# Performance work log

Measured on AMD Instinct MI355X. Metric: run time of the kernel, lower is better.

## Reference

```python
import jax, jax.numpy as jnp
import numpy as np

N_NODES = 100000
N_EDGES = 1000000
D_IN = 256
D_OUT = 64


def setup_inputs() -> dict:
    key = jax.random.key(0)
    k1, k2, k3, k4, k5, k6 = jax.random.split(key, 6)
    x = jax.random.normal(k1, (N_NODES, D_IN), dtype=jnp.float32)
    # Xavier-style uniform init: stdv = 1/sqrt(output_dim)
    stdv = 1.0 / np.sqrt(D_OUT)
    weight = jax.random.uniform(k2, (D_IN, D_OUT), dtype=jnp.float32, minval=-stdv, maxval=stdv)
    adj_vals = jax.random.uniform(k3, (N_EDGES,), dtype=jnp.float32)
    prelu_a = jnp.full((1,), 0.25, dtype=jnp.float32)  # nn.PReLU default
    row = jax.random.randint(k4, (N_EDGES,), 0, N_NODES, dtype=jnp.int32)
    col = jax.random.randint(k5, (N_EDGES,), 0, N_NODES, dtype=jnp.int32)
    return {"x": x, "weight": weight, "adj_vals": adj_vals, "prelu_a": prelu_a,
            "row": row, "col": col}


def reference(x, weight, adj_vals, prelu_a, row, col):
    # dense GEMM: [N, D_in] @ [D_in, D_out]
    hidden = x @ weight  # gc_drop=0 -> identity dropout
    # sparse adj spmm: out[i] = sum_{e: row[e]=i} adj_vals[e] * hidden[col[e]]
    msg = adj_vals[:, None] * hidden[col]  # [E, D_out]
    agg = jax.ops.segment_sum(msg, row, num_segments=N_NODES)  # [N, D_out]
    # PReLU with single shared slope
    out = jnp.where(agg > 0, agg, prelu_a * agg)
    return out
```

## Files before the change

kernel.cpp:

```cpp
#include <hip/hip_runtime.h>

#define N_NODES 100000
#define N_EDGES 1000000
#define D_IN    256
#define D_OUT   64

#define BKT_SHIFT   5
#define NODES_PER_BKT 32
#define N_BKT       3125
#define BKT_CAP     512

#define EPB         2048
#define BIN_BLOCKS  489
#define GEMM_BLOCKS 782
#define NUM_TILES   6250
#define AGG_BLOCKS  391

typedef __attribute__((ext_vector_type(8))) short short8;
typedef __attribute__((ext_vector_type(4))) float f32x4;

__device__ __forceinline__ unsigned short f2bf(float f) {
    unsigned int u = __float_as_uint(f);
    u = (u + 0x7fffu + ((u >> 16) & 1u)) >> 16;
    return (unsigned short)u;
}

__device__ __forceinline__ void mfma_store_tile(
    const short8 afrag[8], const unsigned short wT[64][272],
    unsigned short* __restrict__ hiddenBf, int r0, int n16, int quad)
{
    f32x4 acc[4] = {{0.f,0.f,0.f,0.f},{0.f,0.f,0.f,0.f},
                    {0.f,0.f,0.f,0.f},{0.f,0.f,0.f,0.f}};
#pragma unroll
    for (int ct = 0; ct < 4; ++ct) {
#pragma unroll
        for (int kk = 0; kk < 8; ++kk) {
            short8 b = *(const short8*)&wT[ct * 16 + n16][kk * 32 + quad * 8];
            acc[ct] = __builtin_amdgcn_mfma_f32_16x16x32_bf16(
                afrag[kk], b, acc[ct], 0, 0, 0);
        }
    }
#pragma unroll
    for (int ct = 0; ct < 4; ++ct)
#pragma unroll
        for (int reg = 0; reg < 4; ++reg)
            hiddenBf[(size_t)(r0 + quad * 4 + reg) * D_OUT + ct * 16 + n16]
                = f2bf(acc[ct][reg]);
}

__global__ __launch_bounds__(256, 2) void bin_kernel(
    const int* __restrict__ row, const int* __restrict__ col,
    const float* __restrict__ adj, int* __restrict__ gCursor,
    int2* __restrict__ edges)
{
    __shared__ int cnt[N_BKT];
    __shared__ int cbase[N_BKT];
    __shared__ int cur[N_BKT];

    const int t  = threadIdx.x;
    const int e0 = blockIdx.x * EPB;

    for (int i = t; i < N_BKT; i += 256) cnt[i] = 0;
    __syncthreads();

    int rreg[8];
#pragma unroll
    for (int u = 0; u < 8; ++u) {
        int e = e0 + t + u * 256;
        rreg[u] = (e < N_EDGES) ? row[e] : -1;
    }
#pragma unroll
    for (int u = 0; u < 8; ++u)
        if (rreg[u] >= 0) atomicAdd(&cnt[rreg[u] >> BKT_SHIFT], 1);
    __syncthreads();

    for (int i = t; i < N_BKT; i += 256) {
        int c = cnt[i];
        cbase[i] = c ? atomicAdd(&gCursor[i], c) : 0;
        cur[i] = 0;
    }
    __syncthreads();

    int cc[8]; float vv[8];
#pragma unroll
    for (int u = 0; u < 8; ++u) {
        int e = e0 + t + u * 256;
        if (rreg[u] >= 0) { cc[u] = col[e]; vv[u] = adj[e]; }
        else              { cc[u] = 0;      vv[u] = 0.f;    }
    }
#pragma unroll
    for (int u = 0; u < 8; ++u) {
        int r = rreg[u];
        if (r >= 0) {
            int b = r >> BKT_SHIFT;
            int off = cbase[b] + atomicAdd(&cur[b], 1);
            if (off < BKT_CAP) {
                edges[b * BKT_CAP + off] =
                    make_int2(((r & (NODES_PER_BKT - 1)) << 17) | cc[u],
                              __float_as_int(vv[u]));
            }
        }
    }
}

__global__ __launch_bounds__(256, 2) void gemm_kernel(
    const float* __restrict__ x, const float* __restrict__ w,
    unsigned short* __restrict__ hiddenBf)
{
    const int t = threadIdx.x;

    __shared__ unsigned short wT[64][272];

    for (int i = 0; i < 64; ++i) {
        int idx = t + i * 256;
        int k = idx >> 6, n = idx & 63;
        wT[n][k] = f2bf(w[idx]);
    }
    __syncthreads();

    const int lane = t & 63;
    const int wid  = t >> 6;
    const int n16  = lane & 15;
    const int quad = lane >> 4;

    const int waveGid = blockIdx.x * 4 + wid;
    const int t0 = waveGid * 2;
    if (t0 >= NUM_TILES) return;

    float4 lo[8], hi[8];
    short8 afrag[8];

    {
        const float* xrow = x + (size_t)(t0 * 16 + n16) * D_IN + quad * 8;
#pragma unroll
        for (int kk = 0; kk < 8; ++kk) {
            lo[kk] = *(const float4*)(xrow + kk * 32);
            hi[kk] = *(const float4*)(xrow + kk * 32 + 4);
        }
    }
#pragma unroll
    for (int kk = 0; kk < 8; ++kk) {
        short8 a;
        a[0] = (short)f2bf(lo[kk].x); a[1] = (short)f2bf(lo[kk].y);
        a[2] = (short)f2bf(lo[kk].z); a[3] = (short)f2bf(lo[kk].w);
        a[4] = (short)f2bf(hi[kk].x); a[5] = (short)f2bf(hi[kk].y);
        a[6] = (short)f2bf(hi[kk].z); a[7] = (short)f2bf(hi[kk].w);
        afrag[kk] = a;
    }

    const int t1 = t0 + 1;
    const bool have1 = t1 < NUM_TILES;
    if (have1) {
        const float* xrow = x + (size_t)(t1 * 16 + n16) * D_IN + quad * 8;
#pragma unroll
        for (int kk = 0; kk < 8; ++kk) {
            lo[kk] = *(const float4*)(xrow + kk * 32);
            hi[kk] = *(const float4*)(xrow + kk * 32 + 4);
        }
    }

    mfma_store_tile(afrag, wT, hiddenBf, t0 * 16, n16, quad);

    if (have1) {
#pragma unroll
        for (int kk = 0; kk < 8; ++kk) {
            short8 a;
            a[0] = (short)f2bf(lo[kk].x); a[1] = (short)f2bf(lo[kk].y);
            a[2] = (short)f2bf(lo[kk].z); a[3] = (short)f2bf(lo[kk].w);
            a[4] = (short)f2bf(hi[kk].x); a[5] = (short)f2bf(hi[kk].y);
            a[6] = (short)f2bf(hi[kk].z); a[7] = (short)f2bf(hi[kk].w);
            afrag[kk] = a;
        }
        mfma_store_tile(afrag, wT, hiddenBf, t1 * 16, n16, quad);
    }
}

__global__ __launch_bounds__(512, 2) void bucket_agg_kernel(
    const unsigned short* __restrict__ hiddenBf,
    const int2* __restrict__ edges, const int* __restrict__ gCursor,
    const float* __restrict__ prelu_a, float* __restrict__ out)
{
    __shared__ float acc[8][NODES_PER_BKT * D_OUT];

    const int t      = threadIdx.x;
    const int lane   = t & 63;
    const int wid    = t >> 6;
    const int bucket = blockIdx.x * 8 + wid;
    if (bucket >= N_BKT) return;

    float* A = acc[wid];

    float4* A4 = (float4*)A;
#pragma unroll
    for (int i = 0; i < 8; ++i)
        A4[lane + i * 64] = make_float4(0.f, 0.f, 0.f, 0.f);

    const int base = bucket * BKT_CAP;
    int size = gCursor[bucket];
    if (size > BKT_CAP) size = BKT_CAP;

    for (int i0 = 0; i0 < size; i0 += 64) {
        int take = size - i0;
        if (take > 64) take = 64;
        int2 rec = make_int2(0, 0);
        if (lane < take) rec = edges[base + i0 + lane];

        int j = 0;
        for (; j + 16 <= take; j += 16) {
            int nl[16]; int c[16]; float v[16]; float h[16];
#pragma unroll
            for (int u = 0; u < 16; ++u) {
                int rx = __builtin_amdgcn_readlane(rec.x, j + u);
                nl[u] = (unsigned)rx >> 17;
                c[u]  = rx & 0x1FFFF;
                v[u]  = __int_as_float(__builtin_amdgcn_readlane(rec.y, j + u));
            }
#pragma unroll
            for (int u = 0; u < 16; ++u)
                h[u] = __uint_as_float(
                    (unsigned)hiddenBf[(size_t)c[u] * D_OUT + lane] << 16);
#pragma unroll
            for (int u = 0; u < 16; ++u)
                A[nl[u] * D_OUT + lane] += v[u] * h[u];
        }
        for (; j + 8 <= take; j += 8) {
            int nl[8]; int c[8]; float v[8]; float h[8];
#pragma unroll
            for (int u = 0; u < 8; ++u) {
                int rx = __builtin_amdgcn_readlane(rec.x, j + u);
                nl[u] = (unsigned)rx >> 17;
                c[u]  = rx & 0x1FFFF;
                v[u]  = __int_as_float(__builtin_amdgcn_readlane(rec.y, j + u));
            }
#pragma unroll
            for (int u = 0; u < 8; ++u)
                h[u] = __uint_as_float(
                    (unsigned)hiddenBf[(size_t)c[u] * D_OUT + lane] << 16);
#pragma unroll
            for (int u = 0; u < 8; ++u)
                A[nl[u] * D_OUT + lane] += v[u] * h[u];
        }
        for (; j < take; ++j) {
            int rx  = __builtin_amdgcn_readlane(rec.x, j);
            float v = __int_as_float(__builtin_amdgcn_readlane(rec.y, j));
            float h = __uint_as_float(
                (unsigned)hiddenBf[(size_t)(rx & 0x1FFFF) * D_OUT + lane] << 16);
            A[((unsigned)rx >> 17) * D_OUT + lane] += v * h;
        }
    }

    const float a = prelu_a[0];
    const int node0 = bucket * NODES_PER_BKT;
#pragma unroll
    for (int i = 0; i < NODES_PER_BKT; ++i) {
        float s = A[i * D_OUT + lane];
        out[(size_t)(node0 + i) * D_OUT + lane] = s > 0.f ? s : a * s;
    }
}

extern "C" void kernel_launch(void* const* d_in, const int* in_sizes, int n_in,
                              void* d_out, int out_size, void* d_ws, size_t ws_size,
                              hipStream_t stream)
{
    const float* x       = (const float*)d_in[0];
    const float* w       = (const float*)d_in[1];
    const float* adj     = (const float*)d_in[2];
    const float* prelu_a = (const float*)d_in[3];
    const int*   row     = (const int*)d_in[4];
    const int*   col     = (const int*)d_in[5];
    float* out = (float*)d_out;

    char* ws = (char*)d_ws;
    unsigned short* hiddenBf = (unsigned short*)(ws);
    int2*  edges    = (int2*)        (ws + 12800000);
    int*   gCursor  = (int*)         (ws + 25600000);

    hipMemsetAsync(gCursor, 0, N_BKT * sizeof(int), stream);

    bin_kernel<<<BIN_BLOCKS, 256, 0, stream>>>(row, col, adj, gCursor, edges);

    gemm_kernel<<<GEMM_BLOCKS, 256, 0, stream>>>(x, w, hiddenBf);

    bucket_agg_kernel<<<AGG_BLOCKS, 512, 0, stream>>>(
        hiddenBf, edges, gCursor, prelu_a, out);
}
```

Baseline: 251.9 us.

## Aggregate buckets with MFMA one-hot matmul and fold cursor reset into GEMM

Replaces the per-edge LDS scalar accumulation with a matrix-core formulation. Each wave gathers 32 neighbour rows of bf16 hidden into a transposed LDS tile, builds a one-hot 16x32 edge-to-node matrix holding the edge weight, and accumulates with MFMA. The weight is split into hi and lo bf16 parts to keep precision, which doubles the MFMA count. Buckets shrink to 16 nodes to fit the 16-row MFMA tile. The cursor memset is replaced by zeroing inside the GEMM kernel, which is now launched first.

After: 240.3 us. 4.6% less time.

```diff
diff --git a/kernel.cpp b/kernel.cpp
--- a/kernel.cpp
+++ b/kernel.cpp
@@ -5,19 +5,19 @@
 #define D_IN    256
 #define D_OUT   64
 
-#define BKT_SHIFT   5
-#define NODES_PER_BKT 32
-#define N_BKT       3125
-#define BKT_CAP     512
-
+#define BKT_SHIFT   4
+#define NODES_PER_BKT 16
+#define N_BKT       6250
+#define BKT_CAP     256
 #define EPB         2048
 #define BIN_BLOCKS  489
 #define GEMM_BLOCKS 782
 #define NUM_TILES   6250
-#define AGG_BLOCKS  391
+#define AGG_BLOCKS  782
 
 typedef __attribute__((ext_vector_type(8))) short short8;
 typedef __attribute__((ext_vector_type(4))) float f32x4;
+typedef __attribute__((ext_vector_type(4))) unsigned short u16x4;
 
 __device__ __forceinline__ unsigned short f2bf(float f) {
     unsigned int u = __float_as_uint(f);
@@ -48,66 +48,15 @@
                 = f2bf(acc[ct][reg]);
 }
 
-__global__ __launch_bounds__(256, 2) void bin_kernel(
-    const int* __restrict__ row, const int* __restrict__ col,
-    const float* __restrict__ adj, int* __restrict__ gCursor,
-    int2* __restrict__ edges)
-{
-    __shared__ int cnt[N_BKT];
-    __shared__ int cbase[N_BKT];
-    __shared__ int cur[N_BKT];
-
-    const int t  = threadIdx.x;
-    const int e0 = blockIdx.x * EPB;
-
-    for (int i = t; i < N_BKT; i += 256) cnt[i] = 0;
-    __syncthreads();
-
-    int rreg[8];
-#pragma unroll
-    for (int u = 0; u < 8; ++u) {
-        int e = e0 + t + u * 256;
-        rreg[u] = (e < N_EDGES) ? row[e] : -1;
-    }
-#pragma unroll
-    for (int u = 0; u < 8; ++u)
-        if (rreg[u] >= 0) atomicAdd(&cnt[rreg[u] >> BKT_SHIFT], 1);
-    __syncthreads();
-
-    for (int i = t; i < N_BKT; i += 256) {
-        int c = cnt[i];
-        cbase[i] = c ? atomicAdd(&gCursor[i], c) : 0;
-        cur[i] = 0;
-    }
-    __syncthreads();
-
-    int cc[8]; float vv[8];
-#pragma unroll
-    for (int u = 0; u < 8; ++u) {
-        int e = e0 + t + u * 256;
-        if (rreg[u] >= 0) { cc[u] = col[e]; vv[u] = adj[e]; }
-        else              { cc[u] = 0;      vv[u] = 0.f;    }
-    }
-#pragma unroll
-    for (int u = 0; u < 8; ++u) {
-        int r = rreg[u];
-        if (r >= 0) {
-            int b = r >> BKT_SHIFT;
-            int off = cbase[b] + atomicAdd(&cur[b], 1);
-            if (off < BKT_CAP) {
-                edges[b * BKT_CAP + off] =
-                    make_int2(((r & (NODES_PER_BKT - 1)) << 17) | cc[u],
-                              __float_as_int(vv[u]));
-            }
-        }
-    }
-}
-
 __global__ __launch_bounds__(256, 2) void gemm_kernel(
     const float* __restrict__ x, const float* __restrict__ w,
-    unsigned short* __restrict__ hiddenBf)
+    unsigned short* __restrict__ hiddenBf, int* __restrict__ gCursor)
 {
     const int t = threadIdx.x;
+
+    if (blockIdx.x == 0) {
+        for (int i = t; i < N_BKT; i += 256) gCursor[i] = 0;
+    }
 
     __shared__ unsigned short wT[64][272];
 
@@ -175,25 +124,84 @@
     }
 }
 
-__global__ __launch_bounds__(512, 2) void bucket_agg_kernel(
+__global__ __launch_bounds__(256, 2) void bin_kernel(
+    const int* __restrict__ row, const int* __restrict__ col,
+    const float* __restrict__ adj, int* __restrict__ gCursor,
+    int2* __restrict__ edges)
+{
+    __shared__ int cnt[N_BKT];
+    __shared__ int cbase[N_BKT];
+    __shared__ int cur[N_BKT];
+
+    const int t  = threadIdx.x;
+    const int e0 = blockIdx.x * EPB;
+
+    for (int i = t; i < N_BKT; i += 256) cnt[i] = 0;
+    __syncthreads();
+
+    int rreg[8];
+#pragma unroll
+    for (int u = 0; u < 8; ++u) {
+        int e = e0 + t + u * 256;
+        rreg[u] = (e < N_EDGES) ? row[e] : -1;
+    }
+#pragma unroll
+    for (int u = 0; u < 8; ++u)
+        if (rreg[u] >= 0) atomicAdd(&cnt[rreg[u] >> BKT_SHIFT], 1);
+    __syncthreads();
+
+    for (int i = t; i < N_BKT; i += 256) {
+        int c = cnt[i];
+        cbase[i] = c ? atomicAdd(&gCursor[i], c) : 0;
+        cur[i] = 0;
+    }
+    __syncthreads();
+
+    int cc[8]; float vv[8];
+#pragma unroll
+    for (int u = 0; u < 8; ++u) {
+        int e = e0 + t + u * 256;
+        if (rreg[u] >= 0) { cc[u] = col[e]; vv[u] = adj[e]; }
+        else              { cc[u] = 0;      vv[u] = 0.f;    }
+    }
+#pragma unroll
+    for (int u = 0; u < 8; ++u) {
+        int r = rreg[u];
+        if (r >= 0) {
+            int b = r >> BKT_SHIFT;
+            int off = cbase[b] + atomicAdd(&cur[b], 1);
+            if (off < BKT_CAP) {
+                unsigned hi = f2bf(vv[u]);
+                float hif  = __uint_as_float(hi << 16);
+                unsigned lo = f2bf(vv[u] - hif);
+                edges[b * BKT_CAP + off] =
+                    make_int2(((r & (NODES_PER_BKT - 1)) << 17) | cc[u],
+                              (int)((hi << 16) | lo));
+            }
+        }
+    }
+}
+
+__global__ __launch_bounds__(512) void agg_mfma_kernel(
     const unsigned short* __restrict__ hiddenBf,
     const int2* __restrict__ edges, const int* __restrict__ gCursor,
     const float* __restrict__ prelu_a, float* __restrict__ out)
 {
-    __shared__ float acc[8][NODES_PER_BKT * D_OUT];
-
-    const int t      = threadIdx.x;
-    const int lane   = t & 63;
-    const int wid    = t >> 6;
+    __shared__ unsigned short hT[8][64][40];
+
+    const int t    = threadIdx.x;
+    const int lane = t & 63;
+    const int wid  = t >> 6;
     const int bucket = blockIdx.x * 8 + wid;
     if (bucket >= N_BKT) return;
 
-    float* A = acc[wid];
-
-    float4* A4 = (float4*)A;
-#pragma unroll
-    for (int i = 0; i < 8; ++i)
-        A4[lane + i * 64] = make_float4(0.f, 0.f, 0.f, 0.f);
+    const int n16  = lane & 15;
+    const int quad = lane >> 4;
+
+    unsigned short (*H)[40] = hT[wid];
+
+    f32x4 acc[4] = {{0.f,0.f,0.f,0.f},{0.f,0.f,0.f,0.f},
+                    {0.f,0.f,0.f,0.f},{0.f,0.f,0.f,0.f}};
 
     const int base = bucket * BKT_CAP;
     int size = gCursor[bucket];
@@ -205,57 +213,59 @@
         int2 rec = make_int2(0, 0);
         if (lane < take) rec = edges[base + i0 + lane];
 
-        int j = 0;
-        for (; j + 16 <= take; j += 16) {
-            int nl[16]; int c[16]; float v[16]; float h[16];
-#pragma unroll
-            for (int u = 0; u < 16; ++u) {
-                int rx = __builtin_amdgcn_readlane(rec.x, j + u);
-                nl[u] = (unsigned)rx >> 17;
-                c[u]  = rx & 0x1FFFF;
-                v[u]  = __int_as_float(__builtin_amdgcn_readlane(rec.y, j + u));
-            }
-#pragma unroll
-            for (int u = 0; u < 16; ++u)
-                h[u] = __uint_as_float(
-                    (unsigned)hiddenBf[(size_t)c[u] * D_OUT + lane] << 16);
-#pragma unroll
-            for (int u = 0; u < 16; ++u)
-                A[nl[u] * D_OUT + lane] += v[u] * h[u];
-        }
-        for (; j + 8 <= take; j += 8) {
-            int nl[8]; int c[8]; float v[8]; float h[8];
-#pragma unroll
-            for (int u = 0; u < 8; ++u) {
-                int rx = __builtin_amdgcn_readlane(rec.x, j + u);
-                nl[u] = (unsigned)rx >> 17;
-                c[u]  = rx & 0x1FFFF;
-                v[u]  = __int_as_float(__builtin_amdgcn_readlane(rec.y, j + u));
-            }
-#pragma unroll
-            for (int u = 0; u < 8; ++u)
-                h[u] = __uint_as_float(
-                    (unsigned)hiddenBf[(size_t)c[u] * D_OUT + lane] << 16);
-#pragma unroll
-            for (int u = 0; u < 8; ++u)
-                A[nl[u] * D_OUT + lane] += v[u] * h[u];
-        }
-        for (; j < take; ++j) {
-            int rx  = __builtin_amdgcn_readlane(rec.x, j);
-            float v = __int_as_float(__builtin_amdgcn_readlane(rec.y, j));
-            float h = __uint_as_float(
-                (unsigned)hiddenBf[(size_t)(rx & 0x1FFFF) * D_OUT + lane] << 16);
-            A[((unsigned)rx >> 17) * D_OUT + lane] += v * h;
+#pragma unroll
+        for (int s = 0; s < 2; ++s) {
+#pragma unroll
+            for (int g = 0; g < 2; ++g) {
+                int cc[16]; unsigned short hh[16];
+#pragma unroll
+                for (int u = 0; u < 16; ++u)
+                    cc[u] = __builtin_amdgcn_readlane(rec.x, s * 32 + g * 16 + u)
+                            & 0x1FFFF;
+#pragma unroll
+                for (int u = 0; u < 16; ++u)
+                    hh[u] = hiddenBf[(size_t)cc[u] * D_OUT + lane];
+#pragma unroll
+                for (int u = 0; u < 16; u += 4) {
+                    u16x4 p;
+                    p[0] = hh[u]; p[1] = hh[u + 1];
+                    p[2] = hh[u + 2]; p[3] = hh[u + 3];
+                    *(u16x4*)&H[lane][g * 16 + u] = p;
+                }
+            }
+
+            short8 ahi, alo;
+#pragma unroll
+            for (int j = 0; j < 8; ++j) {
+                int e  = s * 32 + quad * 8 + j;
+                int rx = __shfl(rec.x, e);
+                int ry = __shfl(rec.y, e);
+                bool m = (((unsigned)rx >> 17) == (unsigned)n16);
+                ahi[j] = m ? (short)((unsigned)ry >> 16) : (short)0;
+                alo[j] = m ? (short)(ry & 0xFFFF)        : (short)0;
+            }
+
+#pragma unroll
+            for (int ct = 0; ct < 4; ++ct) {
+                short8 b = *(const short8*)&H[ct * 16 + n16][quad * 8];
+                acc[ct] = __builtin_amdgcn_mfma_f32_16x16x32_bf16(
+                    ahi, b, acc[ct], 0, 0, 0);
+                acc[ct] = __builtin_amdgcn_mfma_f32_16x16x32_bf16(
+                    alo, b, acc[ct], 0, 0, 0);
+            }
         }
     }
 
     const float a = prelu_a[0];
     const int node0 = bucket * NODES_PER_BKT;
 #pragma unroll
-    for (int i = 0; i < NODES_PER_BKT; ++i) {
-        float s = A[i * D_OUT + lane];
-        out[(size_t)(node0 + i) * D_OUT + lane] = s > 0.f ? s : a * s;
-    }
+    for (int ct = 0; ct < 4; ++ct)
+#pragma unroll
+        for (int r = 0; r < 4; ++r) {
+            float sv = acc[ct][r];
+            out[(size_t)(node0 + quad * 4 + r) * D_OUT + ct * 16 + n16]
+                = sv > 0.f ? sv : a * sv;
+        }
 }
 
 extern "C" void kernel_launch(void* const* d_in, const int* in_sizes, int n_in,
@@ -275,12 +285,10 @@
     int2*  edges    = (int2*)        (ws + 12800000);
     int*   gCursor  = (int*)         (ws + 25600000);
 
-    hipMemsetAsync(gCursor, 0, N_BKT * sizeof(int), stream);
+    gemm_kernel<<<GEMM_BLOCKS, 256, 0, stream>>>(x, w, hiddenBf, gCursor);
 
     bin_kernel<<<BIN_BLOCKS, 256, 0, stream>>>(row, col, adj, gCursor, edges);
 
-    gemm_kernel<<<GEMM_BLOCKS, 256, 0, stream>>>(x, w, hiddenBf);
-
-    bucket_agg_kernel<<<AGG_BLOCKS, 512, 0, stream>>>(
+    agg_mfma_kernel<<<AGG_BLOCKS, 512, 0, stream>>>(
         hiddenBf, edges, gCursor, prelu_a, out);
 }
```
